# Kernel optimization log

Measured on AMD Instinct MI355X. Metric: run time of the kernel, lower is better.

## Reference

```python
import jax, jax.numpy as jnp
import numpy as np

D = 1024
H = 16
HD = D // H

def setup_inputs() -> dict:
    key = jax.random.key(0)
    ks = jax.random.split(key, 5)
    scale = 1.0 / np.sqrt(D)
    x = jax.random.normal(ks[0], (2, 2048, D), dtype=jnp.float32)
    W_qkv = jax.random.uniform(ks[1], (D, 3 * D), minval=-scale, maxval=scale, dtype=jnp.float32)
    b_qkv = jax.random.uniform(ks[2], (3 * D,), minval=-scale, maxval=scale, dtype=jnp.float32)
    W_out = jax.random.uniform(ks[3], (D, D), minval=-scale, maxval=scale, dtype=jnp.float32)
    b_out = jax.random.uniform(ks[4], (D,), minval=-scale, maxval=scale, dtype=jnp.float32)
    return {"x": x, "W_qkv": W_qkv, "b_qkv": b_qkv, "W_out": W_out, "b_out": b_out}

def reference(x, W_qkv, b_qkv, W_out, b_out):
    B, S, _ = x.shape
    qkv = x @ W_qkv + b_qkv  # [B,S,3D]
    qkv = qkv.reshape(B, S, 3, H, HD).transpose(2, 0, 3, 1, 4)  # [3,B,H,S,HD]
    q, k, v = qkv[0], qkv[1], qkv[2]
    scores = jnp.einsum('bhsd,bhtd->bhst', q, k) / jnp.sqrt(jnp.float32(HD))
    probs = jax.nn.softmax(scores, axis=-1)
    attn = jnp.einsum('bhst,bhtd->bhsd', probs, v)  # [B,H,S,HD]
    attn = attn.transpose(0, 2, 1, 3).reshape(B, S, D)
    return attn @ W_out + b_out
```

## Files before the change

### kernel.cpp

```cpp
#include <hip/hip_runtime.h>


typedef short bf16x8 __attribute__((ext_vector_type(8)));
typedef float f32x4 __attribute__((ext_vector_type(4)));
typedef unsigned uint2v __attribute__((ext_vector_type(2)));

#define MFMA32(a, b, c) __builtin_amdgcn_mfma_f32_16x16x32_bf16(a, b, c, 0, 0, 0)

__device__ __forceinline__ unsigned short f2bf(float f) {
  unsigned u = __float_as_uint(f);
  u = (u + 0x7fffu + ((u >> 16) & 1u)) >> 16;
  return (unsigned short)u;
}
__device__ __forceinline__ unsigned pack_bf2(float lo, float hi) {
  unsigned a = __float_as_uint(lo) + 0x8000u;
  unsigned b = __float_as_uint(hi) + 0x8000u;
  return __builtin_amdgcn_perm(b, a, 0x07060302);
}
__device__ __forceinline__ void load_lds16(const unsigned short* g, unsigned short* l) {
  __builtin_amdgcn_global_load_lds(
      (const __attribute__((address_space(1))) void*)g,
      (__attribute__((address_space(3))) void*)l, 16, 0, 0);
}

#if __has_builtin(__builtin_amdgcn_permlane32_swap)
__device__ __forceinline__ void pl32_swap(unsigned& a, unsigned& b) {
  uint2v r = __builtin_amdgcn_permlane32_swap(a, b, false, false);
  a = r[0]; b = r[1];
}
__device__ __forceinline__ void pl16_swap(unsigned& a, unsigned& b) {
  uint2v r = __builtin_amdgcn_permlane16_swap(a, b, false, false);
  a = r[0]; b = r[1];
}
#else
__device__ __forceinline__ void pl32_swap(unsigned& a, unsigned& b) {
  asm volatile("s_nop 1\n\tv_permlane32_swap_b32 %0, %1\n\ts_nop 1"
               : "+v"(a), "+v"(b));
}
__device__ __forceinline__ void pl16_swap(unsigned& a, unsigned& b) {
  asm volatile("s_nop 1\n\tv_permlane16_swap_b32 %0, %1\n\ts_nop 1"
               : "+v"(a), "+v"(b));
}
#endif

__global__ __launch_bounds__(256) void prep(
    const float* __restrict__ x, unsigned short* __restrict__ x_bf,
    const float* __restrict__ W_qkv, unsigned short* __restrict__ Wqkv_t,
    const float* __restrict__ W_out, unsigned short* __restrict__ Wout_t)
{
  const int tid = threadIdx.x;
  if (blockIdx.z == 2) {
    const int bid = blockIdx.y * 48 + blockIdx.x;
    const int n = 4096 * 1024;
    for (int i = bid * 2048 + tid * 8; i < n; i += 768 * 2048) {
      float4 f0 = *(const float4*)(x + i);
      float4 f1 = *(const float4*)(x + i + 4);
      union { unsigned short u[8]; uint4 v; } pk;
      pk.u[0] = f2bf(f0.x); pk.u[1] = f2bf(f0.y); pk.u[2] = f2bf(f0.z); pk.u[3] = f2bf(f0.w);
      pk.u[4] = f2bf(f1.x); pk.u[5] = f2bf(f1.y); pk.u[6] = f2bf(f1.z); pk.u[7] = f2bf(f1.w);
      *(uint4*)(x_bf + i) = pk.v;
    }
    return;
  }
  const float* in = (blockIdx.z == 0) ? W_qkv : W_out;
  unsigned short* out = (blockIdx.z == 0) ? Wqkv_t : Wout_t;
  const int R = 1024;
  const int C = (blockIdx.z == 0) ? 3072 : 1024;
  const int c0 = blockIdx.x * 64;
  if (c0 >= C) return;
  __shared__ float tile[64][65];
  const int r0 = blockIdx.y * 64;
  {
    const int rr = tid >> 4;
    const int cc = (tid & 15) * 4;
#pragma unroll
    for (int it = 0; it < 4; ++it) {
      float4 f = *(const float4*)&in[(size_t)(r0 + rr + 16 * it) * C + c0 + cc];
      tile[rr + 16 * it][cc + 0] = f.x;
      tile[rr + 16 * it][cc + 1] = f.y;
      tile[rr + 16 * it][cc + 2] = f.z;
      tile[rr + 16 * it][cc + 3] = f.w;
    }
  }
  __syncthreads();
  {
    const int cr = tid >> 2;
    const int rk = (tid & 3) * 16;
    union { unsigned short u[16]; uint4 v[2]; } pk;
#pragma unroll
    for (int j = 0; j < 16; ++j) pk.u[j] = f2bf(tile[rk + j][cr]);
    uint4* dst = (uint4*)&out[(size_t)(c0 + cr) * R + r0 + rk];
    dst[0] = pk.v[0];
    dst[1] = pk.v[1];
  }
}

template <int MODE, int NB, int BK>
__global__ __launch_bounds__(256) void gemm_mfma(
    const unsigned short* __restrict__ A,
    const unsigned short* __restrict__ Bt,
    const float* __restrict__ bias,
    void* __restrict__ Cout, unsigned short* __restrict__ vT,
    int M, int N, int K, int ldc)
{
  constexpr int NI = NB / 32;
  constexpr int CPR = BK / 8;
  constexpr int RPC = 64 / CPR;
  __shared__ unsigned short As[128][BK];
  __shared__ unsigned short Bs[NB][BK];
  const int tid = threadIdx.x;
  const int wave = tid >> 6, lane = tid & 63;
  const int l16 = lane & 15, quad = lane >> 4;

  const int bid = blockIdx.y * gridDim.x + blockIdx.x;
  const int nwg = gridDim.x * gridDim.y;
  const int sbid = (bid & 7) * (nwg >> 3) + (bid >> 3);
  const int bx = sbid % gridDim.x;
  const int by = sbid / gridDim.x;
  const int m0 = by * 128, n0 = bx * NB;

  const int wm = (wave & 1) * 64, wn = (wave >> 1) * (NB / 2);
  const int lr = lane / CPR;
  const int p  = lane % CPR;
  const int swk = l16 & (CPR - 1);

  f32x4 acc[4][NI] = {};

  for (int k0 = 0; k0 < K; k0 += BK) {
    __syncthreads();
#pragma unroll
    for (int i = 0; i < 32 / RPC; ++i) {
      const int rbase = wave * 32 + i * RPC;
      const int rl = rbase + lr;
      load_lds16(&A[(size_t)(m0 + rl) * K + k0 + ((p ^ (rl & (CPR - 1))) << 3)],
                 &As[rbase][0]);
    }
#pragma unroll
    for (int i = 0; i < (NB / 4) / RPC; ++i) {
      const int rbase = wave * (NB / 4) + i * RPC;
      const int rl = rbase + lr;
      load_lds16(&Bt[(size_t)(n0 + rl) * K + k0 + ((p ^ (rl & (CPR - 1))) << 3)],
                 &Bs[rbase][0]);
    }
    __syncthreads();

#pragma unroll
    for (int kk = 0; kk < BK / 32; ++kk) {
      bf16x8 af[4], bfr[NI];
#pragma unroll
      for (int mi = 0; mi < 4; ++mi)
        af[mi] = *(const bf16x8*)&As[wm + 16 * mi + l16][(((kk << 2) + quad) ^ swk) * 8];
#pragma unroll
      for (int ni = 0; ni < NI; ++ni)
        bfr[ni] = *(const bf16x8*)&Bs[wn + 16 * ni + l16][(((kk << 2) + quad) ^ swk) * 8];
#pragma unroll
      for (int mi = 0; mi < 4; ++mi)
#pragma unroll
        for (int ni = 0; ni < NI; ++ni)
          acc[mi][ni] = __builtin_amdgcn_mfma_f32_16x16x32_bf16(
              af[mi], bfr[ni], acc[mi][ni], 0, 0, 0);
    }
  }

  const float SCQ = 0.18033688f;
#pragma unroll
  for (int ni = 0; ni < NI; ++ni) {
    const int colb = n0 + wn + 16 * ni;
    const int col = colb + l16;
    const float bv = bias[col];
    if (MODE == 0) {
#pragma unroll
      for (int mi = 0; mi < 4; ++mi)
#pragma unroll
        for (int i = 0; i < 4; ++i) {
          const int row = m0 + wm + 16 * mi + quad * 4 + i;
          ((float*)Cout)[(size_t)row * ldc + col] = acc[mi][ni][i] + bv;
        }
    } else if (colb < 1024) {
#pragma unroll
      for (int mi = 0; mi < 4; ++mi)
#pragma unroll
        for (int i = 0; i < 4; ++i) {
          const int row = m0 + wm + 16 * mi + quad * 4 + i;
          ((unsigned short*)Cout)[(size_t)row * ldc + col] = f2bf((acc[mi][ni][i] + bv) * SCQ);
        }
    } else if (colb < 2048) {
#pragma unroll
      for (int mi = 0; mi < 4; ++mi)
#pragma unroll
        for (int i = 0; i < 4; ++i) {
          const int row = m0 + wm + 16 * mi + quad * 4 + i;
          ((unsigned short*)Cout)[(size_t)row * ldc + col] = f2bf(acc[mi][ni][i] + bv);
        }
    } else {
      const int h = (col - 2048) >> 6, d = col & 63;
#pragma unroll
      for (int mi = 0; mi < 4; ++mi) {
        const int row = m0 + wm + 16 * mi + quad * 4;
        const int bb = row >> 11, t = row & 2047;
        unsigned short* dst = &vT[((size_t)(bb * 16 + h) * 64 + d) * 2048 + t];
        *(unsigned*)(dst)     = pack_bf2(acc[mi][ni][0] + bv, acc[mi][ni][1] + bv);
        *(unsigned*)(dst + 2) = pack_bf2(acc[mi][ni][2] + bv, acc[mi][ni][3] + bv);
      }
    }
  }
}

__global__ __launch_bounds__(256, 2) void attn_mfma(
    const unsigned short* __restrict__ qk,
    const unsigned short* __restrict__ vT,
    unsigned short* __restrict__ attn_out)
{
  __shared__ unsigned short Ks[2][4096];
  __shared__ unsigned short Vs[2][4096];

  const int tid = threadIdx.x;
  const int wave = tid >> 6, lane = tid & 63;
  const int l16 = lane & 15, quad = lane >> 4;
  const int bh = blockIdx.y, b = bh >> 4, h = bh & 15;
  const int s0 = blockIdx.x * 128 + wave * 32;

  const unsigned short* qb = qk + (size_t)(b * 2048) * 2048 + h * 64;
  const unsigned short* kb = qb + 1024;
  const unsigned short* vb = vT + (size_t)bh * 64 * 2048;

  const int srow = lane >> 3;
  const int schunk = ((lane & 7) ^ srow) * 8;
  const int r0a = wave * 16;
  const unsigned short* kg0 = kb + (size_t)(r0a + srow) * 2048 + schunk;
  const unsigned short* kg1 = kg0 + (size_t)8 * 2048;
  const unsigned short* vg0 = vb + (size_t)(r0a + srow) * 2048 + schunk;
  const unsigned short* vg1 = vg0 + (size_t)8 * 2048;
  const int wd0 = r0a * 64 + lane * 8;
  const int wd1 = (r0a + 8) * 64 + lane * 8;

  uint4 kr0 = *(const uint4*)(kg0);
  uint4 kr1 = *(const uint4*)(kg1);
  uint4 vr0 = *(const uint4*)(vg0);
  uint4 vr1 = *(const uint4*)(vg1);
  *(uint4*)&Ks[0][wd0] = kr0;  *(uint4*)&Ks[0][wd1] = kr1;
  *(uint4*)&Vs[0][wd0] = vr0;  *(uint4*)&Vs[0][wd1] = vr1;
  kr0 = *(const uint4*)(kg0 + (size_t)64 * 2048);
  kr1 = *(const uint4*)(kg1 + (size_t)64 * 2048);
  vr0 = *(const uint4*)(vg0 + 64);
  vr1 = *(const uint4*)(vg1 + 64);

  bf16x8 qf[2][2];
#pragma unroll
  for (int mt = 0; mt < 2; ++mt)
#pragma unroll
    for (int ks = 0; ks < 2; ++ks)
      qf[mt][ks] = *(const bf16x8*)&qb[(size_t)(s0 + 16 * mt + l16) * 2048 + 32 * ks + quad * 8];

  f32x4 O[2][4] = {};
  f32x4 lacc[2] = {};
  const bf16x8 ones8 = {(short)0x3F80, (short)0x3F80, (short)0x3F80, (short)0x3F80,
                        (short)0x3F80, (short)0x3F80, (short)0x3F80, (short)0x3F80};
  const int sw = l16 & 7;

  __syncthreads();

  for (int it = 0; it < 32; ++it) {
    const int cur = it & 1;

    bf16x8 kf[4][2];
#pragma unroll
    for (int nt = 0; nt < 4; ++nt) {
      const int rb = (16 * nt + l16) * 64;
      kf[nt][0] = *(const bf16x8*)&Ks[cur][rb + ((quad ^ sw) * 8)];
      kf[nt][1] = *(const bf16x8*)&Ks[cur][rb + (((4 + quad) ^ sw) * 8)];
    }

    f32x4 sf[4][2];
#pragma unroll
    for (int nt = 0; nt < 4; ++nt)
#pragma unroll
      for (int mt = 0; mt < 2; ++mt) {
        f32x4 c = {0.0f, 0.0f, 0.0f, 0.0f};
        c = __builtin_amdgcn_mfma_f32_16x16x32_bf16(kf[nt][0], qf[mt][0], c, 0, 0, 0);
        c = __builtin_amdgcn_mfma_f32_16x16x32_bf16(kf[nt][1], qf[mt][1], c, 0, 0, 0);
        sf[nt][mt] = c;
      }

    if (it < 31) {
      *(uint4*)&Ks[cur ^ 1][wd0] = kr0;
      *(uint4*)&Ks[cur ^ 1][wd1] = kr1;
      *(uint4*)&Vs[cur ^ 1][wd0] = vr0;
      *(uint4*)&Vs[cur ^ 1][wd1] = vr1;
      if (it < 30) {
        const size_t ko = (size_t)(it + 2) * 64 * 2048;
        kr0 = *(const uint4*)(kg0 + ko);
        kr1 = *(const uint4*)(kg1 + ko);
        vr0 = *(const uint4*)(vg0 + (it + 2) * 64);
        vr1 = *(const uint4*)(vg1 + (it + 2) * 64);
      }
    }

    bf16x8 vf[4][2];
#pragma unroll
    for (int nd = 0; nd < 4; ++nd) {
      const int rb = (16 * nd + l16) * 64;
      vf[nd][0] = *(const bf16x8*)&Vs[cur][rb + ((quad ^ sw) * 8)];
      vf[nd][1] = *(const bf16x8*)&Vs[cur][rb + (((4 + quad) ^ sw) * 8)];
    }

    bf16x8 pB[2][2];
#pragma unroll
    for (int mt = 0; mt < 2; ++mt)
#pragma unroll
      for (int c = 0; c < 2; ++c) {
        const f32x4 sa = sf[2 * c][mt];
        const f32x4 sb = sf[2 * c + 1][mt];
        unsigned X = pack_bf2(__builtin_amdgcn_exp2f(sa[0]), __builtin_amdgcn_exp2f(sa[1]));
        unsigned Y = pack_bf2(__builtin_amdgcn_exp2f(sa[2]), __builtin_amdgcn_exp2f(sa[3]));
        unsigned Z = pack_bf2(__builtin_amdgcn_exp2f(sb[0]), __builtin_amdgcn_exp2f(sb[1]));
        unsigned W = pack_bf2(__builtin_amdgcn_exp2f(sb[2]), __builtin_amdgcn_exp2f(sb[3]));
        pl32_swap(X, Z);
        pl16_swap(X, Z);
        pl32_swap(Y, W);
        pl16_swap(Y, W);
        union { unsigned u[4]; bf16x8 v; } pk;
        pk.u[0] = X; pk.u[1] = Y; pk.u[2] = Z; pk.u[3] = W;
        pB[mt][c] = pk.v;
      }

#pragma unroll
    for (int c = 0; c < 2; ++c)
#pragma unroll
      for (int mt = 0; mt < 2; ++mt) {
        lacc[mt] = MFMA32(ones8, pB[mt][c], lacc[mt]);
#pragma unroll
        for (int nd = 0; nd < 4; ++nd)
          O[mt][nd] = MFMA32(vf[nd][c], pB[mt][c], O[mt][nd]);
      }

    __syncthreads();
  }

#pragma unroll
  for (int mt = 0; mt < 2; ++mt) {
    const float inv = 1.0f / lacc[mt][0];
    const size_t row = (size_t)(b * 2048 + s0 + 16 * mt + l16);
#pragma unroll
    for (int nd = 0; nd < 4; ++nd) {
      uint2 w;
      w.x = pack_bf2(O[mt][nd][0] * inv, O[mt][nd][1] * inv);
      w.y = pack_bf2(O[mt][nd][2] * inv, O[mt][nd][3] * inv);
      *(uint2*)&attn_out[row * 1024 + h * 64 + 16 * nd + quad * 4] = w;
    }
  }
}

extern "C" void kernel_launch(void* const* d_in, const int* in_sizes, int n_in,
                              void* d_out, int out_size, void* d_ws, size_t ws_size,
                              hipStream_t stream) {
  const float* x     = (const float*)d_in[0];
  const float* W_qkv = (const float*)d_in[1];
  const float* b_qkv = (const float*)d_in[2];
  const float* W_out = (const float*)d_in[3];
  const float* b_out = (const float*)d_in[4];
  float* out = (float*)d_out;

  char* ws = (char*)d_ws;
  const size_t MB = 1048576;
  unsigned short* Wout_t = (unsigned short*)(ws);
  unsigned short* qk_bf  = (unsigned short*)(ws + 2 * MB);
  unsigned short* vT     = (unsigned short*)(ws + 18 * MB);
  unsigned short* attn_b = (unsigned short*)(ws + 26 * MB);
  unsigned short* x_bf   = (unsigned short*)(ws + 34 * MB);
  unsigned short* Wqkv_t = (unsigned short*)(ws + 42 * MB);

  prep<<<dim3(48, 16, 3), 256, 0, stream>>>(x, x_bf, W_qkv, Wqkv_t, W_out, Wout_t);

  gemm_mfma<1, 192, 64><<<dim3(16, 32), 256, 0, stream>>>(x_bf, Wqkv_t, b_qkv, qk_bf, vT,
                                                          4096, 3072, 1024, 2048);
  attn_mfma<<<dim3(16, 32), 256, 0, stream>>>(qk_bf, vT, attn_b);
  gemm_mfma<0, 64, 64><<<dim3(16, 32), 256, 0, stream>>>(attn_b, Wout_t, b_out, out, nullptr,
                                                         4096, 1024, 1024, 1024);
}
```

Measured before the change: 180.2 us.

## Process two KV tiles per barrier with doubled LDS staging in attention

The attention loop now stages two 64-key K/V tiles per shared-memory buffer and runs 16 iterations instead of 32. Each iteration computes both sub-tiles between barriers, and two sets of register prefetches stay in flight. This halves the number of __syncthreads and gives more memory latency hiding. In exchange, LDS use doubles to 64KB per block and register pressure rises, which may reduce occupancy under launch_bounds(256,2).

```diff
diff --git a/kernel.cpp b/kernel.cpp
--- a/kernel.cpp
+++ b/kernel.cpp
@@ -211,8 +211,8 @@
     const unsigned short* __restrict__ vT,
     unsigned short* __restrict__ attn_out)
 {
-  __shared__ unsigned short Ks[2][4096];
-  __shared__ unsigned short Vs[2][4096];
+  __shared__ unsigned short Ks[2][2][4096];
+  __shared__ unsigned short Vs[2][2][4096];
 
   const int tid = threadIdx.x;
   const int wave = tid >> 6, lane = tid & 63;
@@ -238,12 +238,22 @@
   uint4 kr1 = *(const uint4*)(kg1);
   uint4 vr0 = *(const uint4*)(vg0);
   uint4 vr1 = *(const uint4*)(vg1);
-  *(uint4*)&Ks[0][wd0] = kr0;  *(uint4*)&Ks[0][wd1] = kr1;
-  *(uint4*)&Vs[0][wd0] = vr0;  *(uint4*)&Vs[0][wd1] = vr1;
+  *(uint4*)&Ks[0][0][wd0] = kr0;  *(uint4*)&Ks[0][0][wd1] = kr1;
+  *(uint4*)&Vs[0][0][wd0] = vr0;  *(uint4*)&Vs[0][0][wd1] = vr1;
   kr0 = *(const uint4*)(kg0 + (size_t)64 * 2048);
   kr1 = *(const uint4*)(kg1 + (size_t)64 * 2048);
   vr0 = *(const uint4*)(vg0 + 64);
   vr1 = *(const uint4*)(vg1 + 64);
+  *(uint4*)&Ks[0][1][wd0] = kr0;  *(uint4*)&Ks[0][1][wd1] = kr1;
+  *(uint4*)&Vs[0][1][wd0] = vr0;  *(uint4*)&Vs[0][1][wd1] = vr1;
+  kr0 = *(const uint4*)(kg0 + (size_t)2 * 64 * 2048);
+  kr1 = *(const uint4*)(kg1 + (size_t)2 * 64 * 2048);
+  vr0 = *(const uint4*)(vg0 + 128);
+  vr1 = *(const uint4*)(vg1 + 128);
+  uint4 kr2 = *(const uint4*)(kg0 + (size_t)3 * 64 * 2048);
+  uint4 kr3 = *(const uint4*)(kg1 + (size_t)3 * 64 * 2048);
+  uint4 vr2 = *(const uint4*)(vg0 + 192);
+  uint4 vr3 = *(const uint4*)(vg1 + 192);
 
   bf16x8 qf[2][2];
 #pragma unroll
@@ -260,79 +270,96 @@
 
   __syncthreads();
 
-  for (int it = 0; it < 32; ++it) {
+  for (int it = 0; it < 16; ++it) {
     const int cur = it & 1;
 
-    bf16x8 kf[4][2];
-#pragma unroll
-    for (int nt = 0; nt < 4; ++nt) {
-      const int rb = (16 * nt + l16) * 64;
-      kf[nt][0] = *(const bf16x8*)&Ks[cur][rb + ((quad ^ sw) * 8)];
-      kf[nt][1] = *(const bf16x8*)&Ks[cur][rb + (((4 + quad) ^ sw) * 8)];
-    }
-
-    f32x4 sf[4][2];
-#pragma unroll
-    for (int nt = 0; nt < 4; ++nt)
-#pragma unroll
-      for (int mt = 0; mt < 2; ++mt) {
-        f32x4 c = {0.0f, 0.0f, 0.0f, 0.0f};
-        c = __builtin_amdgcn_mfma_f32_16x16x32_bf16(kf[nt][0], qf[mt][0], c, 0, 0, 0);
-        c = __builtin_amdgcn_mfma_f32_16x16x32_bf16(kf[nt][1], qf[mt][1], c, 0, 0, 0);
-        sf[nt][mt] = c;
+#pragma unroll
+    for (int s = 0; s < 2; ++s) {
+      bf16x8 kf[4][2];
+#pragma unroll
+      for (int nt = 0; nt < 4; ++nt) {
+        const int rb = (16 * nt + l16) * 64;
+        kf[nt][0] = *(const bf16x8*)&Ks[cur][s][rb + ((quad ^ sw) * 8)];
+        kf[nt][1] = *(const bf16x8*)&Ks[cur][s][rb + (((4 + quad) ^ sw) * 8)];
       }
 
-    if (it < 31) {
-      *(uint4*)&Ks[cur ^ 1][wd0] = kr0;
-      *(uint4*)&Ks[cur ^ 1][wd1] = kr1;
-      *(uint4*)&Vs[cur ^ 1][wd0] = vr0;
-      *(uint4*)&Vs[cur ^ 1][wd1] = vr1;
-      if (it < 30) {
-        const size_t ko = (size_t)(it + 2) * 64 * 2048;
-        kr0 = *(const uint4*)(kg0 + ko);
-        kr1 = *(const uint4*)(kg1 + ko);
-        vr0 = *(const uint4*)(vg0 + (it + 2) * 64);
-        vr1 = *(const uint4*)(vg1 + (it + 2) * 64);
+      f32x4 sf[4][2];
+#pragma unroll
+      for (int nt = 0; nt < 4; ++nt)
+#pragma unroll
+        for (int mt = 0; mt < 2; ++mt) {
+          f32x4 c = {0.0f, 0.0f, 0.0f, 0.0f};
+          c = __builtin_amdgcn_mfma_f32_16x16x32_bf16(kf[nt][0], qf[mt][0], c, 0, 0, 0);
+          c = __builtin_amdgcn_mfma_f32_16x16x32_bf16(kf[nt][1], qf[mt][1], c, 0, 0, 0);
+          sf[nt][mt] = c;
+        }
+
+      if (it < 15) {
+        if (s == 0) {
+          *(uint4*)&Ks[cur ^ 1][0][wd0] = kr0;
+          *(uint4*)&Ks[cur ^ 1][0][wd1] = kr1;
+          *(uint4*)&Vs[cur ^ 1][0][wd0] = vr0;
+          *(uint4*)&Vs[cur ^ 1][0][wd1] = vr1;
+          if (it < 14) {
+            const size_t ko = (size_t)(2 * it + 4) * 64 * 2048;
+            kr0 = *(const uint4*)(kg0 + ko);
+            kr1 = *(const uint4*)(kg1 + ko);
+            vr0 = *(const uint4*)(vg0 + (2 * it + 4) * 64);
+            vr1 = *(const uint4*)(vg1 + (2 * it + 4) * 64);
+          }
+        } else {
+          *(uint4*)&Ks[cur ^ 1][1][wd0] = kr2;
+          *(uint4*)&Ks[cur ^ 1][1][wd1] = kr3;
+          *(uint4*)&Vs[cur ^ 1][1][wd0] = vr2;
+          *(uint4*)&Vs[cur ^ 1][1][wd1] = vr3;
+          if (it < 14) {
+            const size_t ko = (size_t)(2 * it + 5) * 64 * 2048;
+            kr2 = *(const uint4*)(kg0 + ko);
+            kr3 = *(const uint4*)(kg1 + ko);
+            vr2 = *(const uint4*)(vg0 + (2 * it + 5) * 64);
+            vr3 = *(const uint4*)(vg1 + (2 * it + 5) * 64);
+          }
+        }
       }
-    }
-
-    bf16x8 vf[4][2];
-#pragma unroll
-    for (int nd = 0; nd < 4; ++nd) {
-      const int rb = (16 * nd + l16) * 64;
-      vf[nd][0] = *(const bf16x8*)&Vs[cur][rb + ((quad ^ sw) * 8)];
-      vf[nd][1] = *(const bf16x8*)&Vs[cur][rb + (((4 + quad) ^ sw) * 8)];
-    }
-
-    bf16x8 pB[2][2];
-#pragma unroll
-    for (int mt = 0; mt < 2; ++mt)
-#pragma unroll
-      for (int c = 0; c < 2; ++c) {
-        const f32x4 sa = sf[2 * c][mt];
-        const f32x4 sb = sf[2 * c + 1][mt];
-        unsigned X = pack_bf2(__builtin_amdgcn_exp2f(sa[0]), __builtin_amdgcn_exp2f(sa[1]));
-        unsigned Y = pack_bf2(__builtin_amdgcn_exp2f(sa[2]), __builtin_amdgcn_exp2f(sa[3]));
-        unsigned Z = pack_bf2(__builtin_amdgcn_exp2f(sb[0]), __builtin_amdgcn_exp2f(sb[1]));
-        unsigned W = pack_bf2(__builtin_amdgcn_exp2f(sb[2]), __builtin_amdgcn_exp2f(sb[3]));
-        pl32_swap(X, Z);
-        pl16_swap(X, Z);
-        pl32_swap(Y, W);
-        pl16_swap(Y, W);
-        union { unsigned u[4]; bf16x8 v; } pk;
-        pk.u[0] = X; pk.u[1] = Y; pk.u[2] = Z; pk.u[3] = W;
-        pB[mt][c] = pk.v;
+
+      bf16x8 vf[4][2];
+#pragma unroll
+      for (int nd = 0; nd < 4; ++nd) {
+        const int rb = (16 * nd + l16) * 64;
+        vf[nd][0] = *(const bf16x8*)&Vs[cur][s][rb + ((quad ^ sw) * 8)];
+        vf[nd][1] = *(const bf16x8*)&Vs[cur][s][rb + (((4 + quad) ^ sw) * 8)];
       }
 
-#pragma unroll
-    for (int c = 0; c < 2; ++c)
-#pragma unroll
-      for (int mt = 0; mt < 2; ++mt) {
-        lacc[mt] = MFMA32(ones8, pB[mt][c], lacc[mt]);
-#pragma unroll
-        for (int nd = 0; nd < 4; ++nd)
-          O[mt][nd] = MFMA32(vf[nd][c], pB[mt][c], O[mt][nd]);
-      }
+      bf16x8 pB[2][2];
+#pragma unroll
+      for (int mt = 0; mt < 2; ++mt)
+#pragma unroll
+        for (int c = 0; c < 2; ++c) {
+          const f32x4 sa = sf[2 * c][mt];
+          const f32x4 sb = sf[2 * c + 1][mt];
+          unsigned X = pack_bf2(__builtin_amdgcn_exp2f(sa[0]), __builtin_amdgcn_exp2f(sa[1]));
+          unsigned Y = pack_bf2(__builtin_amdgcn_exp2f(sa[2]), __builtin_amdgcn_exp2f(sa[3]));
+          unsigned Z = pack_bf2(__builtin_amdgcn_exp2f(sb[0]), __builtin_amdgcn_exp2f(sb[1]));
+          unsigned W = pack_bf2(__builtin_amdgcn_exp2f(sb[2]), __builtin_amdgcn_exp2f(sb[3]));
+          pl32_swap(X, Z);
+          pl16_swap(X, Z);
+          pl32_swap(Y, W);
+          pl16_swap(Y, W);
+          union { unsigned u[4]; bf16x8 v; } pk;
+          pk.u[0] = X; pk.u[1] = Y; pk.u[2] = Z; pk.u[3] = W;
+          pB[mt][c] = pk.v;
+        }
+
+#pragma unroll
+      for (int c = 0; c < 2; ++c)
+#pragma unroll
+        for (int mt = 0; mt < 2; ++mt) {
+          lacc[mt] = MFMA32(ones8, pB[mt][c], lacc[mt]);
+#pragma unroll
+          for (int nd = 0; nd < 4; ++nd)
+            O[mt][nd] = MFMA32(vf[nd][c], pB[mt][c], O[mt][nd]);
+        }
+    }
 
     __syncthreads();
   }
```

New measurement: 178.6 us. About the same (-0.9%).
